# Kernel optimization log

Measured on AMD Instinct MI355X. Metric: run time of the kernel, lower is better.

Reference implementation:

```python
import jax, jax.numpy as jnp
import numpy as np

EMBED_DIM = 1024
NUM_HEADS = 16
HEAD_DIM = EMBED_DIM // NUM_HEADS
B, T, S = 2, 2048, 2048


def setup_inputs() -> dict:
    key = jax.random.key(0)
    ks = jax.random.split(key, 12)
    xavier = lambda k: jax.random.uniform(k, (EMBED_DIM, EMBED_DIM), jnp.float32,
                                          -np.sqrt(6.0 / (2 * EMBED_DIM)), np.sqrt(6.0 / (2 * EMBED_DIM)))
    return {
        "query": jax.random.normal(ks[0], (B, T, EMBED_DIM), jnp.float32),
        "key": jax.random.normal(ks[1], (B, S, EMBED_DIM), jnp.float32),
        "value": jax.random.normal(ks[2], (B, S, EMBED_DIM), jnp.float32),
        "key_padding_mask": jnp.zeros((B, S), dtype=bool),  # False = keep
        "Wq": xavier(ks[3]), "bq": jnp.zeros((EMBED_DIM,), jnp.float32),
        "Wk": xavier(ks[4]), "bk": jnp.zeros((EMBED_DIM,), jnp.float32),
        "Wv": xavier(ks[5]), "bv": jnp.zeros((EMBED_DIM,), jnp.float32),
        "Wo": xavier(ks[6]), "bo": jnp.zeros((EMBED_DIM,), jnp.float32),
    }


def reference(query, key, value, key_padding_mask, Wq, bq, Wk, bk, Wv, bv, Wo, bo):
    bsz, tgt_len, _ = query.shape
    src_len = key.shape[1]
    # projections (torch Linear: x @ W.T + b)
    q = (query @ Wq.T + bq).reshape(bsz, tgt_len, NUM_HEADS, HEAD_DIM).transpose(0, 2, 1, 3)
    k = (key @ Wk.T + bk).reshape(bsz, src_len, NUM_HEADS, HEAD_DIM).transpose(0, 2, 1, 3)
    v = (value @ Wv.T + bv).reshape(bsz, src_len, NUM_HEADS, HEAD_DIM).transpose(0, 2, 1, 3)
    scale = HEAD_DIM ** (-0.5)
    # [B, H, T, S] attention scores
    scores = jnp.einsum("bhtd,bhsd->bhts", q, k) * scale
    # causal mask (causal=True path)
    causal_mask = jnp.triu(jnp.ones((tgt_len, src_len), dtype=bool), k=1)
    neg_inf = jnp.finfo(scores.dtype).min
    scores = jnp.where(causal_mask[None, None], neg_inf, scores)
    # key padding mask: True = masked out
    scores = jnp.where(key_padding_mask[:, None, None, :], neg_inf, scores)
    attn = jax.nn.softmax(scores, axis=-1)
    # dropout p=0.0 (eval) -> identity
    out = jnp.einsum("bhts,bhsd->bhtd", attn, v)
    out = out.transpose(0, 2, 1, 3).reshape(bsz, tgt_len, EMBED_DIM)
    return out @ Wo.T + bo
```

## Files before the change

kernel.cpp:

```cpp
#include <hip/hip_runtime.h>
#include <stdint.h>
#include <stddef.h>


typedef __attribute__((ext_vector_type(8))) short short8;
typedef __attribute__((ext_vector_type(4))) float f32x4;

#define QSCALE (0.125f * 1.4426950408889634f)
#define NEG_BIG (-3.0e38f)

static __device__ __forceinline__ unsigned short f2bf(float f) {
  unsigned int u = __builtin_bit_cast(unsigned int, f);
  u += 0x7fffu + ((u >> 16) & 1u);
  return (unsigned short)(u >> 16);
}

static __device__ __forceinline__ void async_g2l16(const void* g, void* l) {
  __builtin_amdgcn_global_load_lds((const __attribute__((address_space(1))) void*)g,
                                   (__attribute__((address_space(3))) void*)l,
                                   16, 0, 0);
}

struct CvtArgs { const float* s[7]; unsigned short* d[7]; int nblk[7]; };

__global__ __launch_bounds__(256) void cvt(CvtArgs a) {
  const int z = blockIdx.z;
  if ((int)blockIdx.x >= a.nblk[z]) return;
  const float* __restrict__ s = a.s[z];
  unsigned short* __restrict__ d = a.d[z];
  const size_t i = ((size_t)blockIdx.x * 256 + threadIdx.x) * 8;
  float4 v0 = *(const float4*)(s + i);
  float4 v1 = *(const float4*)(s + i + 4);
  short8 o = {(short)f2bf(v0.x), (short)f2bf(v0.y), (short)f2bf(v0.z), (short)f2bf(v0.w),
              (short)f2bf(v1.x), (short)f2bf(v1.y), (short)f2bf(v1.z), (short)f2bf(v1.w)};
  *(short8*)(d + i) = o;
}

constexpr int GK = 1024;
constexpr int GN = 1024;

struct GemmArgs {
  const void* A[3];
  const unsigned short* W[3];
  const float* bias[3];
  void* out[3];
  float scale[3];
};

template <int MT, int BN, bool A_BF16, bool OUT_F32>
__global__ __launch_bounds__(256) void gemm_bt(GemmArgs args) {
  constexpr int ROWS = MT * 32;
  constexpr int NT = BN / 32;
  const int z = blockIdx.z;
  const unsigned short* __restrict__ W = args.W[z];
  const float* __restrict__ bias = args.bias[z];
  const float scale = args.scale[z];

  const int m0 = blockIdx.x * ROWS;
  const int n0 = blockIdx.y * BN;

  __shared__ __attribute__((aligned(16))) short As[2][ROWS * 64];
  __shared__ __attribute__((aligned(16))) short Bs[2][BN * 64];

  const int tid = threadIdx.x;
  const int lane = tid & 63;
  const int w = tid >> 6;
  const int quad = lane >> 4;
  const int l15 = lane & 15;
  const int wm = w >> 1, wn = w & 1;

  auto stage = [&](int buf, int k0) {
#pragma unroll
    for (int it = 0; it < BN / 32; ++it) {
      const int c = it * 256 + tid;
      const int row = c >> 3, cc = c & 7;
      const int gcc = cc ^ (row & 7);
      async_g2l16(W + (size_t)(n0 + row) * GK + k0 + gcc * 8, &Bs[buf][c * 8]);
    }
    if constexpr (A_BF16) {
#pragma unroll
      for (int it = 0; it < ROWS / 32; ++it) {
        const int c = it * 256 + tid;
        const int row = c >> 3, cc = c & 7;
        const int gcc = cc ^ (row & 7);
        async_g2l16((const unsigned short*)args.A[z] + (size_t)(m0 + row) * GK + k0 + gcc * 8,
                    &As[buf][c * 8]);
      }
    } else {
      const int sr = tid >> 1;
      const int sh = tid & 1;
      const float* ga = (const float*)args.A[z] + (size_t)(m0 + sr) * GK + k0;
      short* la = &As[buf][sr * 64];
#pragma unroll
      for (int i = 0; i < 4; ++i) {
        const int cc = sh * 4 + i;
        const int gcc = cc ^ (sr & 7);
        float4 v0 = *(const float4*)(ga + gcc * 8);
        float4 v1 = *(const float4*)(ga + gcc * 8 + 4);
        short8 o = {(short)f2bf(v0.x), (short)f2bf(v0.y), (short)f2bf(v0.z), (short)f2bf(v0.w),
                    (short)f2bf(v1.x), (short)f2bf(v1.y), (short)f2bf(v1.z), (short)f2bf(v1.w)};
        *(short8*)(la + cc * 8) = o;
      }
    }
  };

  f32x4 acc[MT][NT];
#pragma unroll
  for (int i = 0; i < MT; ++i)
#pragma unroll
    for (int j = 0; j < NT; ++j)
      acc[i][j] = (f32x4){0.f, 0.f, 0.f, 0.f};

  stage(0, 0);
  __syncthreads();

  int cur = 0;
  for (int k0 = 0; k0 < GK; k0 += 64) {
    if (k0 + 64 < GK) stage(cur ^ 1, k0 + 64);

#pragma unroll
    for (int kh = 0; kh < 2; ++kh) {
      short8 af[MT], bfr[NT];
#pragma unroll
      for (int mt = 0; mt < MT; ++mt) {
        const int r = wm * (MT * 16) + mt * 16 + l15;
        af[mt] = *(const short8*)(&As[cur][0] + r * 64 + ((kh * 4 + quad) ^ (r & 7)) * 8);
      }
#pragma unroll
      for (int nt = 0; nt < NT; ++nt) {
        const int r = wn * (BN / 2) + nt * 16 + l15;
        bfr[nt] = *(const short8*)(&Bs[cur][0] + r * 64 + ((kh * 4 + quad) ^ (r & 7)) * 8);
      }
#pragma unroll
      for (int mt = 0; mt < MT; ++mt)
#pragma unroll
        for (int nt = 0; nt < NT; ++nt)
          acc[mt][nt] = __builtin_amdgcn_mfma_f32_16x16x32_bf16(af[mt], bfr[nt], acc[mt][nt], 0, 0, 0);
    }

    __syncthreads();
    cur ^= 1;
  }

  float bv[NT];
#pragma unroll
  for (int nt = 0; nt < NT; ++nt)
    bv[nt] = bias[n0 + wn * (BN / 2) + nt * 16 + l15];

#pragma unroll
  for (int mt = 0; mt < MT; ++mt) {
    const int mbase = m0 + wm * (MT * 16) + mt * 16 + quad * 4;
#pragma unroll
    for (int nt = 0; nt < NT; ++nt) {
      const int n = n0 + wn * (BN / 2) + nt * 16 + l15;
#pragma unroll
      for (int r = 0; r < 4; ++r) {
        const float v = (acc[mt][nt][r] + bv[nt]) * scale;
        if constexpr (OUT_F32)
          ((float*)args.out[z])[(size_t)(mbase + r) * GN + n] = v;
        else
          ((unsigned short*)args.out[z])[(size_t)(mbase + r) * GN + n] = f2bf(v);
      }
    }
  }
}

constexpr int AT = 2048, ASL = 2048, AE = 1024;

__global__ __launch_bounds__(256, 3) void attn(const unsigned short* Q,
                                               const unsigned short* __restrict__ K,
                                               const unsigned short* __restrict__ V,
                                               unsigned short* O) {
  const int bid = blockIdx.x;
  const int bh = bid & 31;
  const int j = bid >> 5;
  const int qt = (j < 8) ? 31 - j : (j < 16) ? j - 8 : (j < 24) ? 39 - j : j - 16;
  const int b = bh >> 4;
  const int h = bh & 15;
  const int qbase = qt * 64;

  const int tid = threadIdx.x;
  const int lane = tid & 63;
  const int w = tid >> 6;
  const int quad = lane >> 4;
  const int l15 = lane & 15;
  const int wq = w & 1;
  const int ws = w >> 1;

  const unsigned short* Qb = Q + (size_t)b * AT * AE + (size_t)h * 64;
  const unsigned short* Kb = K + (size_t)b * ASL * AE + (size_t)h * 64;
  const unsigned short* Vb = V + (size_t)b * ASL * AE + (size_t)h * 64;
  unsigned short* Ob = O + (size_t)b * AT * AE + (size_t)h * 64;

  __shared__ __attribute__((aligned(16))) char pool[52224];
  short* Ks = (short*)pool;
  unsigned int* Vt = (unsigned int*)(pool + 16384);
  short* Ps = (short*)(pool + 33792);
  float* Ep = (float*)pool;

  short8 qf[2][2];
#pragma unroll
  for (int mt = 0; mt < 2; ++mt) {
    const unsigned short* qrow = Qb + (size_t)(qbase + wq * 32 + mt * 16 + l15) * AE + quad * 8;
    qf[mt][0] = *(const short8*)qrow;
    qf[mt][1] = *(const short8*)(qrow + 32);
  }

  f32x4 oacc[2][4];
  float lrow[2][4];
#pragma unroll
  for (int mt = 0; mt < 2; ++mt) {
#pragma unroll
    for (int d = 0; d < 4; ++d) oacc[mt][d] = (f32x4){0.f, 0.f, 0.f, 0.f};
#pragma unroll
    for (int r = 0; r < 4; ++r) lrow[mt][r] = 0.f;
  }

  for (int s0 = 0; s0 <= qbase; s0 += 128) {
    const int rem = qbase + 64 - s0;
    __syncthreads();
#pragma unroll
    for (int it = 0; it < 4; ++it) {
      const int u = it * 256 + tid;
      const int r = u >> 3, c = u & 7;
      if (r < rem)
        async_g2l16(Kb + (size_t)(s0 + r) * AE + ((c ^ (r & 7)) * 8), Ks + u * 8);
    }
#pragma unroll
    for (int it = 0; it < 2; ++it) {
      const int t = it * 256 + tid;
      const int spv = t >> 3, ckv = t & 7;
      if (2 * spv < rem) {
        const short8 va = *(const short8*)(Vb + (size_t)(s0 + 2 * spv) * AE + ckv * 8);
        const short8 vb2 = *(const short8*)(Vb + (size_t)(s0 + 2 * spv + 1) * AE + ckv * 8);
        const int spi = spv ^ (ckv * 4);
#pragma unroll
        for (int jj = 0; jj < 8; ++jj) {
          const unsigned int pk = (unsigned int)(unsigned short)va[jj] |
                                  ((unsigned int)(unsigned short)vb2[jj] << 16);
          Vt[(ckv * 8 + jj) * 68 + spi] = pk;
        }
      }
    }
    __syncthreads();

    const int ssub = s0 + ws * 64;
    if (ssub <= qbase + wq * 32 + 31) {
      short8 kb0[4], kb1[4];
#pragma unroll
      for (int ct = 0; ct < 4; ++ct) {
        const int r = ws * 64 + ct * 16 + l15;
        const short* base = Ks + r * 64;
        kb0[ct] = *(const short8*)(base + ((quad ^ (r & 7)) * 8));
        kb1[ct] = *(const short8*)(base + (((4 + quad) ^ (r & 7)) * 8));
      }

      f32x4 sc[2][4];
#pragma unroll
      for (int mt = 0; mt < 2; ++mt)
#pragma unroll
        for (int ct = 0; ct < 4; ++ct) sc[mt][ct] = (f32x4){0.f, 0.f, 0.f, 0.f};
      __builtin_amdgcn_s_setprio(1);
#pragma unroll
      for (int mt = 0; mt < 2; ++mt)
#pragma unroll
        for (int ct = 0; ct < 4; ++ct) {
          sc[mt][ct] = __builtin_amdgcn_mfma_f32_16x16x32_bf16(qf[mt][0], kb0[ct], sc[mt][ct], 0, 0, 0);
          sc[mt][ct] = __builtin_amdgcn_mfma_f32_16x16x32_bf16(qf[mt][1], kb1[ct], sc[mt][ct], 0, 0, 0);
        }
      __builtin_amdgcn_s_setprio(0);

#pragma unroll
      for (int mt = 0; mt < 2; ++mt) {
        const int qm0 = qbase + wq * 32 + mt * 16;
        if (ssub + 63 > qm0) {
          const int trow = qm0 + quad * 4;
#pragma unroll
          for (int ct = 0; ct < 4; ++ct) {
            const int sg = ssub + ct * 16 + l15;
#pragma unroll
            for (int r = 0; r < 4; ++r)
              sc[mt][ct][r] = (sg <= trow + r) ? sc[mt][ct][r] : NEG_BIG;
          }
        }
      }

#pragma unroll
      for (int mt = 0; mt < 2; ++mt) {
        short* Pw = Ps + (w * 2 + mt) * (16 * 72);
#pragma unroll
        for (int ct = 0; ct < 4; ++ct)
#pragma unroll
          for (int r = 0; r < 4; ++r) {
            const unsigned int u =
                __builtin_bit_cast(unsigned int, __builtin_amdgcn_exp2f(sc[mt][ct][r]));
            lrow[mt][r] += __builtin_bit_cast(float, u & 0xffff0000u);
            Pw[(quad * 4 + r) * 72 + ct * 16 + l15] = (short)(u >> 16);
          }
      }
      asm volatile("s_waitcnt lgkmcnt(0)" ::: "memory");
      __builtin_amdgcn_sched_barrier(0);

      short8 pf[2][2];
#pragma unroll
      for (int mt = 0; mt < 2; ++mt) {
        const short* Pw = Ps + (w * 2 + mt) * (16 * 72);
        pf[mt][0] = *(const short8*)(Pw + l15 * 72 + quad * 8);
        pf[mt][1] = *(const short8*)(Pw + l15 * 72 + 32 + quad * 8);
      }
      short8 vf0[4], vf1[4];
#pragma unroll
      for (int d = 0; d < 4; ++d) {
        const int dd = d * 16 + l15;
        const int ck4 = ((dd >> 3) & 7) * 4;
        const unsigned int* row = Vt + dd * 68 + ws * 32;
        vf0[d] = *(const short8*)(row + ((quad * 4) ^ ck4));
        vf1[d] = *(const short8*)(row + ((16 + quad * 4) ^ ck4));
      }
      __builtin_amdgcn_s_setprio(1);
#pragma unroll
      for (int mt = 0; mt < 2; ++mt)
#pragma unroll
        for (int d = 0; d < 4; ++d) {
          oacc[mt][d] = __builtin_amdgcn_mfma_f32_16x16x32_bf16(pf[mt][0], vf0[d], oacc[mt][d], 0, 0, 0);
          oacc[mt][d] = __builtin_amdgcn_mfma_f32_16x16x32_bf16(pf[mt][1], vf1[d], oacc[mt][d], 0, 0, 0);
        }
      __builtin_amdgcn_s_setprio(0);
    }
  }

  float red[2][4];
#pragma unroll
  for (int mt = 0; mt < 2; ++mt)
#pragma unroll
    for (int r = 0; r < 4; ++r) {
      float v = lrow[mt][r];
#pragma unroll
      for (int off = 1; off < 16; off <<= 1)
        v += __shfl_xor(v, off, 64);
      red[mt][r] = v;
    }

  __syncthreads();
  float* Epq = Ep + wq * (32 * 68);
  if (ws == 1) {
#pragma unroll
    for (int mt = 0; mt < 2; ++mt) {
#pragma unroll
      for (int d = 0; d < 4; ++d)
#pragma unroll
        for (int r = 0; r < 4; ++r)
          Epq[(mt * 16 + quad * 4 + r) * 68 + d * 16 + l15] = oacc[mt][d][r];
      if (l15 == 0) {
#pragma unroll
        for (int r = 0; r < 4; ++r)
          Epq[(mt * 16 + quad * 4 + r) * 68 + 64] = red[mt][r];
      }
    }
  }
  __syncthreads();
  if (ws == 0) {
#pragma unroll
    for (int mt = 0; mt < 2; ++mt)
#pragma unroll
      for (int r = 0; r < 4; ++r) {
        const int ql = mt * 16 + quad * 4 + r;
        const float lsum = red[mt][r] + Epq[ql * 68 + 64];
        const float inv = 1.0f / fmaxf(lsum, 1e-30f);
        const int t = qbase + wq * 32 + ql;
#pragma unroll
        for (int d = 0; d < 4; ++d)
          Ob[(size_t)t * AE + d * 16 + l15] =
              f2bf((oacc[mt][d][r] + Epq[ql * 68 + d * 16 + l15]) * inv);
      }
  }
}

extern "C" void kernel_launch(void* const* d_in, const int* in_sizes, int n_in,
                              void* d_out, int out_size, void* d_ws, size_t ws_size,
                              hipStream_t stream) {
  const float* query = (const float*)d_in[0];
  const float* key   = (const float*)d_in[1];
  const float* value = (const float*)d_in[2];
  const float* Wq = (const float*)d_in[4];
  const float* bq = (const float*)d_in[5];
  const float* Wk = (const float*)d_in[6];
  const float* bk = (const float*)d_in[7];
  const float* Wv = (const float*)d_in[8];
  const float* bv = (const float*)d_in[9];
  const float* Wo = (const float*)d_in[10];
  const float* bo = (const float*)d_in[11];

  const size_t NQ = (size_t)4096 * 1024;
  const size_t NW = (size_t)1024 * 1024;

  unsigned short* Qp = (unsigned short*)d_ws;
  unsigned short* Kp = Qp + NQ;
  unsigned short* Vp = Kp + NQ;

  const bool big = ws_size >= (3 * NQ + 3 * NQ + 4 * NW) * 2;

  if (big) {
    unsigned short* Qi  = Vp + NQ;
    unsigned short* Ki  = Qi + NQ;
    unsigned short* Vi  = Ki + NQ;
    unsigned short* Wqb = Vi + NQ;
    unsigned short* Wkb = Wqb + NW;
    unsigned short* Wvb = Wkb + NW;
    unsigned short* Wob = Wvb + NW;

    CvtArgs ca;
    ca.s[0] = query; ca.d[0] = Qi;  ca.nblk[0] = 2048;
    ca.s[1] = key;   ca.d[1] = Ki;  ca.nblk[1] = 2048;
    ca.s[2] = value; ca.d[2] = Vi;  ca.nblk[2] = 2048;
    ca.s[3] = Wq;    ca.d[3] = Wqb; ca.nblk[3] = 512;
    ca.s[4] = Wk;    ca.d[4] = Wkb; ca.nblk[4] = 512;
    ca.s[5] = Wv;    ca.d[5] = Wvb; ca.nblk[5] = 512;
    ca.s[6] = Wo;    ca.d[6] = Wob; ca.nblk[6] = 512;
    cvt<<<dim3(2048, 1, 7), 256, 0, stream>>>(ca);

    GemmArgs ga;
    ga.A[0] = Qi; ga.W[0] = Wqb; ga.bias[0] = bq; ga.out[0] = Qp; ga.scale[0] = QSCALE;
    ga.A[1] = Ki; ga.W[1] = Wkb; ga.bias[1] = bk; ga.out[1] = Kp; ga.scale[1] = 1.0f;
    ga.A[2] = Vi; ga.W[2] = Wvb; ga.bias[2] = bv; ga.out[2] = Vp; ga.scale[2] = 1.0f;
    gemm_bt<4, 128, true, false><<<dim3(32, 8, 3), 256, 0, stream>>>(ga);

    attn<<<dim3(1024), 256, 0, stream>>>(Qp, Kp, Vp, Qp);

    GemmArgs go;
    go.A[0] = Qp; go.W[0] = Wob; go.bias[0] = bo; go.out[0] = d_out; go.scale[0] = 1.0f;
    go.A[1] = nullptr; go.W[1] = nullptr; go.bias[1] = nullptr; go.out[1] = nullptr; go.scale[1] = 1.0f;
    go.A[2] = nullptr; go.W[2] = nullptr; go.bias[2] = nullptr; go.out[2] = nullptr; go.scale[2] = 1.0f;
    gemm_bt<2, 64, true, true><<<dim3(64, 16, 1), 256, 0, stream>>>(go);
  } else {
    unsigned short* Wqb = Vp + NQ;
    unsigned short* Wkb = Wqb + NW;
    unsigned short* Wvb = Wkb + NW;
    unsigned short* Wob = Wvb + NW;

    CvtArgs ca;
    ca.s[0] = Wq; ca.d[0] = Wqb; ca.nblk[0] = 512;
    ca.s[1] = Wk; ca.d[1] = Wkb; ca.nblk[1] = 512;
    ca.s[2] = Wv; ca.d[2] = Wvb; ca.nblk[2] = 512;
    ca.s[3] = Wo; ca.d[3] = Wob; ca.nblk[3] = 512;
    ca.s[4] = nullptr; ca.d[4] = nullptr; ca.nblk[4] = 0;
    ca.s[5] = nullptr; ca.d[5] = nullptr; ca.nblk[5] = 0;
    ca.s[6] = nullptr; ca.d[6] = nullptr; ca.nblk[6] = 0;
    cvt<<<dim3(512, 1, 4), 256, 0, stream>>>(ca);

    GemmArgs ga;
    ga.A[0] = query; ga.W[0] = Wqb; ga.bias[0] = bq; ga.out[0] = Qp; ga.scale[0] = QSCALE;
    ga.A[1] = key;   ga.W[1] = Wkb; ga.bias[1] = bk; ga.out[1] = Kp; ga.scale[1] = 1.0f;
    ga.A[2] = value; ga.W[2] = Wvb; ga.bias[2] = bv; ga.out[2] = Vp; ga.scale[2] = 1.0f;
    gemm_bt<4, 128, false, false><<<dim3(32, 8, 3), 256, 0, stream>>>(ga);

    attn<<<dim3(1024), 256, 0, stream>>>(Qp, Kp, Vp, Qp);

    GemmArgs go;
    go.A[0] = Qp; go.W[0] = Wob; go.bias[0] = bo; go.out[0] = d_out; go.scale[0] = 1.0f;
    go.A[1] = nullptr; go.W[1] = nullptr; go.bias[1] = nullptr; go.out[1] = nullptr; go.scale[1] = 1.0f;
    go.A[2] = nullptr; go.W[2] = nullptr; go.bias[2] = nullptr; go.out[2] = nullptr; go.scale[2] = 1.0f;
    gemm_bt<2, 64, true, true><<<dim3(64, 16, 1), 256, 0, stream>>>(go);
  }
}
```

Baseline: 208.8 us.

## Add triple-buffered async-LDS QKV projection GEMM with swizzled tiles

Replaces the generic templated GEMM used for the fused Q/K/V projections with a dedicated 128x128 tile kernel. It stages tiles straight from global memory into LDS through a three-deep ring, using XOR-swizzled columns to avoid bank conflicts, and waits on partial vmcnt so two tiles stay in flight while the current one is computed. The goal is to hide global load latency and cut LDS conflicts in the projection stage. In exchange it uses more shared memory per block (about 96KB), which may lower occupancy.

```diff
diff --git a/kernel.cpp b/kernel.cpp
--- a/kernel.cpp
+++ b/kernel.cpp
@@ -46,6 +46,115 @@
   void* out[3];
   float scale[3];
 };
+
+__global__ __launch_bounds__(256) void gemm_qkv(GemmArgs args) {
+  constexpr int ROWS = 128, BN = 128;
+  const int z = blockIdx.z;
+  const unsigned short* __restrict__ A = (const unsigned short*)args.A[z];
+  const unsigned short* __restrict__ W = args.W[z];
+  const float* __restrict__ bias = args.bias[z];
+  const float scale = args.scale[z];
+  const int m0 = blockIdx.x * ROWS;
+  const int n0 = blockIdx.y * BN;
+
+  __shared__ __attribute__((aligned(16))) short As[3][ROWS * 64];
+  __shared__ __attribute__((aligned(16))) short Bs[3][BN * 64];
+
+  const int tid = threadIdx.x;
+  const int lane = tid & 63;
+  const int w = tid >> 6;
+  const int quad = lane >> 4;
+  const int l15 = lane & 15;
+  const int wm = w >> 1, wn = w & 1;
+
+  auto stage = [&](int buf, int k0) {
+#pragma unroll
+    for (int it = 0; it < 4; ++it) {
+      const int c = it * 256 + tid;
+      const int row = c >> 3, cc = c & 7;
+      const int gcc = cc ^ (row & 7);
+      async_g2l16(W + (size_t)(n0 + row) * GK + k0 + gcc * 8, &Bs[buf][c * 8]);
+    }
+#pragma unroll
+    for (int it = 0; it < 4; ++it) {
+      const int c = it * 256 + tid;
+      const int row = c >> 3, cc = c & 7;
+      const int gcc = cc ^ (row & 7);
+      async_g2l16(A + (size_t)(m0 + row) * GK + k0 + gcc * 8, &As[buf][c * 8]);
+    }
+  };
+
+  f32x4 acc[4][4];
+#pragma unroll
+  for (int i = 0; i < 4; ++i)
+#pragma unroll
+    for (int j = 0; j < 4; ++j)
+      acc[i][j] = (f32x4){0.f, 0.f, 0.f, 0.f};
+
+  auto compute = [&](int buf) {
+#pragma unroll
+    for (int kh = 0; kh < 2; ++kh) {
+      short8 af[4], bfr[4];
+#pragma unroll
+      for (int mt = 0; mt < 4; ++mt) {
+        const int r = wm * 64 + mt * 16 + l15;
+        af[mt] = *(const short8*)(&As[buf][0] + r * 64 + ((kh * 4 + quad) ^ (r & 7)) * 8);
+      }
+#pragma unroll
+      for (int nt = 0; nt < 4; ++nt) {
+        const int r = wn * 64 + nt * 16 + l15;
+        bfr[nt] = *(const short8*)(&Bs[buf][0] + r * 64 + ((kh * 4 + quad) ^ (r & 7)) * 8);
+      }
+#pragma unroll
+      for (int mt = 0; mt < 4; ++mt)
+#pragma unroll
+        for (int nt = 0; nt < 4; ++nt)
+          acc[mt][nt] = __builtin_amdgcn_mfma_f32_16x16x32_bf16(af[mt], bfr[nt], acc[mt][nt], 0, 0, 0);
+    }
+  };
+
+  stage(0, 0);
+  stage(1, 64);
+
+  int bc = 0, bs = 2;
+  for (int k = 0; k < 14; ++k) {
+    asm volatile("s_waitcnt vmcnt(8)" ::: "memory");
+    __builtin_amdgcn_sched_barrier(0);
+    __builtin_amdgcn_s_barrier();
+    stage(bs, (k + 2) * 64);
+    compute(bc);
+    bc = (bc == 2) ? 0 : bc + 1;
+    bs = (bs == 2) ? 0 : bs + 1;
+  }
+  asm volatile("s_waitcnt vmcnt(8)" ::: "memory");
+  __builtin_amdgcn_sched_barrier(0);
+  __builtin_amdgcn_s_barrier();
+  compute(bc);
+  bc = (bc == 2) ? 0 : bc + 1;
+  asm volatile("s_waitcnt vmcnt(0)" ::: "memory");
+  __builtin_amdgcn_sched_barrier(0);
+  __builtin_amdgcn_s_barrier();
+  compute(bc);
+
+  float bv[4];
+#pragma unroll
+  for (int nt = 0; nt < 4; ++nt)
+    bv[nt] = bias[n0 + wn * 64 + nt * 16 + l15];
+
+#pragma unroll
+  for (int mt = 0; mt < 4; ++mt) {
+    const int mbase = m0 + wm * 64 + mt * 16 + quad * 4;
+#pragma unroll
+    for (int nt = 0; nt < 4; ++nt) {
+      const int n = n0 + wn * 64 + nt * 16 + l15;
+#pragma unroll
+      for (int r = 0; r < 4; ++r) {
+        const float v = (acc[mt][nt][r] + bv[nt]) * scale;
+        ((unsigned short*)args.out[z])[(size_t)(mbase + r) * GN + n] = f2bf(v);
+      }
+    }
+  }
+}
 
 template <int MT, int BN, bool A_BF16, bool OUT_F32>
 __global__ __launch_bounds__(256) void gemm_bt(GemmArgs args) {
@@ -423,7 +532,7 @@
     ga.A[0] = Qi; ga.W[0] = Wqb; ga.bias[0] = bq; ga.out[0] = Qp; ga.scale[0] = QSCALE;
     ga.A[1] = Ki; ga.W[1] = Wkb; ga.bias[1] = bk; ga.out[1] = Kp; ga.scale[1] = 1.0f;
     ga.A[2] = Vi; ga.W[2] = Wvb; ga.bias[2] = bv; ga.out[2] = Vp; ga.scale[2] = 1.0f;
-    gemm_bt<4, 128, true, false><<<dim3(32, 8, 3), 256, 0, stream>>>(ga);
+    gemm_qkv<<<dim3(32, 8, 3), 256, 0, stream>>>(ga);
 
     attn<<<dim3(1024), 256, 0, stream>>>(Qp, Kp, Vp, Qp);
 
```

After: 223.7 us. +7.2%, slower.
